# Kernel optimization log

Hardware: AMD Instinct MI355X
Metric: run time of the kernel (lower is better)

Reference implementation:

```python
import jax, jax.numpy as jnp
import numpy as np

N_TAPS = 16
BATCH = 64
T = 480000  # 10 s @ 48 kHz, divisible by hop_length=256


def setup_inputs() -> dict:
    key = jax.random.key(0)
    k1, k2 = jax.random.split(key)
    x = jax.random.normal(k1, (BATCH, T), dtype=jnp.float32)
    b = jax.random.normal(k2, (N_TAPS,), dtype=jnp.float32) * 0.1
    return {"x": x, "b": b}


def reference(x, b):
    """Causal FIR filter: y[t] = sum_k b[k] * x[t-k], zero initial state.

    Equivalent to the torch module's per-timestep shift-register loop,
    expressed as one batched 1-D cross-correlation.
    """
    n = b.shape[0]
    # left-pad with n-1 zeros == zero-initialized shift register
    xp = jnp.pad(x, ((0, 0), (n - 1, 0)))[:, None, :]  # [B, 1, T+n-1]
    # lax.conv is cross-correlation; flip taps so w matches y[t]=sum b[k] x[t-k]
    w = b[::-1][None, None, :]  # [out=1, in=1, width=n]
    y = jax.lax.conv_general_dilated(
        xp, w, window_strides=(1,), padding='VALID',
        dimension_numbers=('NCH', 'OIH', 'NCH'))
    return y[:, 0, :]  # [B, T]
```

## Files before the change

kernel.cpp:

```cpp
#include <hip/hip_runtime.h>

#define BATCH 64
#define T 480000
#define T4 (T / 4)
#define NTAPS 16

__global__ __launch_bounds__(256) void fir_apply_kernel(
    const float* __restrict__ x,
    const float* __restrict__ b,
    float* __restrict__ y)
{
    const int gid = blockIdx.x * blockDim.x + threadIdx.x;
    if (gid >= BATCH * T4) return;

    const int row  = gid / T4;
    const int col4 = gid - row * T4;

    const float4* xr = (const float4*)(x + (size_t)row * T);

    float s[20];
#pragma unroll
    for (int m = 0; m < 5; ++m) {
        const int c = col4 - 4 + m;
        float4 v;
        if (c >= 0) {
            v = xr[c];
        } else {
            v = make_float4(0.f, 0.f, 0.f, 0.f);
        }
        s[4 * m + 0] = v.x;
        s[4 * m + 1] = v.y;
        s[4 * m + 2] = v.z;
        s[4 * m + 3] = v.w;
    }

    float tap[NTAPS];
#pragma unroll
    for (int k = 0; k < NTAPS; ++k) tap[k] = b[k];

    float acc[4];
#pragma unroll
    for (int j = 0; j < 4; ++j) {
        float a = 0.f;
#pragma unroll
        for (int k = 0; k < NTAPS; ++k) {
            a += tap[k] * s[16 + j - k];
        }
        acc[j] = a;
    }

    float4* yr = (float4*)(y + (size_t)row * T);
    yr[col4] = make_float4(acc[0], acc[1], acc[2], acc[3]);
}

extern "C" void kernel_launch(void* const* d_in, const int* in_sizes, int n_in,
                              void* d_out, int out_size, void* d_ws, size_t ws_size,
                              hipStream_t stream)
{
    const float* x = (const float*)d_in[0];
    const float* b = (const float*)d_in[1];
    float* y = (float*)d_out;

    const int total4 = BATCH * T4;
    const int block = 256;
    const int grid = (total4 + block - 1) / block;

    fir_apply_kernel<<<grid, block, 0, stream>>>(x, b, y);
}
```

Baseline: 222.3 us.

## Use grid-stride loop with software-prefetched loads and nontemporal stores

Replaces the one-thread-per-float4 launch with a fixed 2048-block grid-stride loop that prefetches the next iteration's five float4 loads while computing the current one. Output is written with nontemporal stores, and the boundary branch becomes a clamped load followed by a select. The goal is to hide memory latency, amortize the tap loads across iterations, and keep output from polluting cache. In exchange it raises register pressure and lowers the number of resident waves.

```diff
diff --git a/kernel.cpp b/kernel.cpp
--- a/kernel.cpp
+++ b/kernel.cpp
@@ -4,53 +4,79 @@
 #define T 480000
 #define T4 (T / 4)
 #define NTAPS 16
+#define NC (BATCH * T4)
+
+typedef float floatx4 __attribute__((ext_vector_type(4)));
+
+__device__ __forceinline__ void load5(const float* __restrict__ x, int idx,
+                                      floatx4 v[5])
+{
+    const unsigned row  = (unsigned)idx / (unsigned)T4;
+    const int      col4 = idx - (int)(row * T4);
+    const floatx4* xr   = (const floatx4*)(x + (size_t)row * T);
+#pragma unroll
+    for (int m = 0; m < 5; ++m) {
+        const int c  = col4 - 4 + m;
+        const int cc = c < 0 ? 0 : c;
+        floatx4 t = xr[cc];
+        if (c < 0) t = (floatx4){0.f, 0.f, 0.f, 0.f};
+        v[m] = t;
+    }
+}
 
 __global__ __launch_bounds__(256) void fir_apply_kernel(
     const float* __restrict__ x,
     const float* __restrict__ b,
     float* __restrict__ y)
 {
-    const int gid = blockIdx.x * blockDim.x + threadIdx.x;
-    if (gid >= BATCH * T4) return;
-
-    const int row  = gid / T4;
-    const int col4 = gid - row * T4;
-
-    const float4* xr = (const float4*)(x + (size_t)row * T);
-
-    float s[20];
-#pragma unroll
-    for (int m = 0; m < 5; ++m) {
-        const int c = col4 - 4 + m;
-        float4 v;
-        if (c >= 0) {
-            v = xr[c];
-        } else {
-            v = make_float4(0.f, 0.f, 0.f, 0.f);
-        }
-        s[4 * m + 0] = v.x;
-        s[4 * m + 1] = v.y;
-        s[4 * m + 2] = v.z;
-        s[4 * m + 3] = v.w;
-    }
-
     float tap[NTAPS];
 #pragma unroll
     for (int k = 0; k < NTAPS; ++k) tap[k] = b[k];
 
-    float acc[4];
+    const int stride = gridDim.x * blockDim.x;
+    int idx = blockIdx.x * blockDim.x + threadIdx.x;
+    if (idx >= NC) return;
+
+    floatx4* yv = (floatx4*)y;
+
+    floatx4 v[5];
+    load5(x, idx, v);
+
+    for (;;) {
+        const int nidx = idx + stride;
+        const bool have_next = nidx < NC;
+
+        floatx4 w[5];
+        if (have_next) load5(x, nidx, w);
+
+        float s[20];
 #pragma unroll
-    for (int j = 0; j < 4; ++j) {
-        float a = 0.f;
+        for (int m = 0; m < 5; ++m) {
+            s[4 * m + 0] = v[m].x;
+            s[4 * m + 1] = v[m].y;
+            s[4 * m + 2] = v[m].z;
+            s[4 * m + 3] = v[m].w;
+        }
+
+        float acc[4];
 #pragma unroll
-        for (int k = 0; k < NTAPS; ++k) {
-            a += tap[k] * s[16 + j - k];
+        for (int j = 0; j < 4; ++j) {
+            float a = 0.f;
+#pragma unroll
+            for (int k = 0; k < NTAPS; ++k) {
+                a += tap[k] * s[16 + j - k];
+            }
+            acc[j] = a;
         }
-        acc[j] = a;
+
+        floatx4 out = {acc[0], acc[1], acc[2], acc[3]};
+        __builtin_nontemporal_store(out, yv + idx);
+
+        if (!have_next) break;
+#pragma unroll
+        for (int m = 0; m < 5; ++m) v[m] = w[m];
+        idx = nidx;
     }
-
-    float4* yr = (float4*)(y + (size_t)row * T);
-    yr[col4] = make_float4(acc[0], acc[1], acc[2], acc[3]);
 }
 
 extern "C" void kernel_launch(void* const* d_in, const int* in_sizes, int n_in,
@@ -61,9 +87,8 @@
     const float* b = (const float*)d_in[1];
     float* y = (float*)d_out;
 
-    const int total4 = BATCH * T4;
     const int block = 256;
-    const int grid = (total4 + block - 1) / block;
+    const int grid = 2048;
 
     fir_apply_kernel<<<grid, block, 0, stream>>>(x, b, y);
 }
```

After: 215.6 us. 3.0% less time.
